# Kernel tuning notes

Hardware: AMD Instinct MI355X
Metric: run time of the kernel (lower is better)

Reference implementation:

```python
import jax, jax.numpy as jnp
import numpy as np

N = 50000      # nodes
E = 800000     # edges (avg degree 16)
IN, H, OUT = 128, 256, 2
BN_EPS = 1e-5


def setup_inputs() -> dict:
    key = jax.random.key(0)
    ks = jax.random.split(key, 24)
    w = lambda k, s: jax.random.normal(k, s, jnp.float32) * 0.05
    inp = {
        "x": jax.random.normal(ks[0], (N, IN), jnp.float32),
        "edge_index": jax.random.randint(ks[1], (2, E), 0, N, jnp.int64),
    }
    # GINConv 1 MLP: Linear(IN,H) -> BN(H) -> ReLU -> Linear(H,H) -> ReLU
    inp.update(c1_W1=w(ks[2], (IN, H)), c1_b1=w(ks[3], (H,)),
               c1_g=jnp.ones((H,), jnp.float32), c1_be=jnp.zeros((H,), jnp.float32),
               c1_W2=w(ks[4], (H, H)), c1_b2=w(ks[5], (H,)))
    # GINConv 2
    inp.update(c2_W1=w(ks[6], (H, H)), c2_b1=w(ks[7], (H,)),
               c2_g=jnp.ones((H,), jnp.float32), c2_be=jnp.zeros((H,), jnp.float32),
               c2_W2=w(ks[8], (H, H)), c2_b2=w(ks[9], (H,)))
    # GINConv 3
    inp.update(c3_W1=w(ks[10], (H, H)), c3_b1=w(ks[11], (H,)),
               c3_g=jnp.ones((H,), jnp.float32), c3_be=jnp.zeros((H,), jnp.float32),
               c3_W2=w(ks[12], (H, H)), c3_b2=w(ks[13], (H,)))
    # readout head
    inp.update(lin1_W=w(ks[14], (3 * H, 3 * H)), lin1_b=w(ks[15], (3 * H,)),
               lin2_W=w(ks[16], (3 * H, OUT)), lin2_b=w(ks[17], (OUT,)))
    return inp


def _gin_conv(x, src, dst, W1, b1, g, be, W2, b2):
    # sum-aggregate neighbor features: agg[i] = sum_{e: dst[e]==i} x[src[e]]
    agg = jax.ops.segment_sum(x[src], dst, num_segments=N)
    h = (x + agg) @ W1 + b1            # (1+eps)*x + agg, eps=0
    mu = h.mean(axis=0)
    var = h.var(axis=0)                # biased var, as torch BN training
    h = jax.nn.relu((h - mu) * jax.lax.rsqrt(var + BN_EPS) * g + be)
    return jax.nn.relu(h @ W2 + b2)


def reference(x, edge_index,
              c1_W1, c1_b1, c1_g, c1_be, c1_W2, c1_b2,
              c2_W1, c2_b1, c2_g, c2_be, c2_W2, c2_b2,
              c3_W1, c3_b1, c3_g, c3_be, c3_W2, c3_b2,
              lin1_W, lin1_b, lin2_W, lin2_b):
    src, dst = edge_index[0], edge_index[1]
    h1 = _gin_conv(x, src, dst, c1_W1, c1_b1, c1_g, c1_be, c1_W2, c1_b2)
    h2 = _gin_conv(h1, src, dst, c2_W1, c2_b1, c2_g, c2_be, c2_W2, c2_b2)
    h3 = _gin_conv(h2, src, dst, c3_W1, c3_b1, c3_g, c3_be, c3_W2, c3_b2)
    h = jnp.concatenate((h1, h2, h3), axis=1)        # [N, 3H]
    h = jax.nn.relu(h @ lin1_W + lin1_b)
    h = h @ lin2_W + lin2_b                          # [N, OUT]
    return h, jax.nn.softmax(h, axis=1)
```

## Files before the change

kernel.cpp:

```cpp
#include <hip/hip_runtime.h>
#include <hip/hip_bf16.h>


#define GIN_N_FEAT_IN 128
#define GIN_H 256
#define M_PAD_ROWS 50176

typedef short short8 __attribute__((ext_vector_type(8)));
typedef float f32x4 __attribute__((ext_vector_type(4)));

#define SCHED_FENCE() __builtin_amdgcn_sched_barrier(0)
#define RAW_BARRIER() __builtin_amdgcn_s_barrier()

__device__ inline ushort f32_to_bf16(float f) {
    union { float f; uint u; } x; x.f = f;
    uint r = x.u + 0x7fff + ((x.u >> 16) & 1);
    return (ushort)(r >> 16);
}
__device__ inline float bf16_to_f32(uint h) {
    union { uint u; float f; } x; x.u = h << 16;
    return x.f;
}
__device__ inline uint pack_bf16(float lo, float hi) {
    return (uint)f32_to_bf16(lo) | ((uint)f32_to_bf16(hi) << 16);
}

__device__ inline void gload_lds16(const ushort* g, ushort* l) {
    __builtin_amdgcn_global_load_lds(
        (const __attribute__((address_space(1))) void*)g,
        (__attribute__((address_space(3))) void*)l, 16, 0, 0);
}


__global__ void cvt_f32_bf16(const float* __restrict__ in, ushort* __restrict__ out, int npairs) {
    for (int i = blockIdx.x * blockDim.x + threadIdx.x; i < npairs; i += gridDim.x * blockDim.x) {
        float2 v = ((const float2*)in)[i];
        ((uint*)out)[i] = pack_bf16(v.x, v.y);
    }
}

struct WPrep {
    const float* src[7];
    ushort* dst[7];
    int R[7];
    int C[7];
};

__global__ void prep_weights(WPrep p) {
    int which = blockIdx.y;
    int R = p.R[which], C = p.C[which];
    int total = R * C;
    const float* src = p.src[which];
    ushort* dst = p.dst[which];
    for (int idx = blockIdx.x * blockDim.x + threadIdx.x; idx < total;
         idx += gridDim.x * blockDim.x) {
        int r = idx / C, c = idx - r * C;
        dst[(size_t)c * R + r] = f32_to_bf16(src[idx]);
    }
}


__global__ void count_kernel(const int* __restrict__ ei, int* __restrict__ deg, int E) {
    for (int e = blockIdx.x * blockDim.x + threadIdx.x; e < E; e += gridDim.x * blockDim.x) {
        atomicAdd(&deg[ei[E + e]], 1);
    }
}

__global__ void scan_chunk(const int* __restrict__ deg, int* __restrict__ row_start,
                           int* __restrict__ chunk_sums, int N) {
    __shared__ int sm[256];
    int tid = threadIdx.x;
    int idx = blockIdx.x * 256 + tid;
    int v = (idx < N) ? deg[idx] : 0;
    sm[tid] = v;
    __syncthreads();
    #pragma unroll
    for (int off = 1; off < 256; off <<= 1) {
        int t = (tid >= off) ? sm[tid - off] : 0;
        __syncthreads();
        sm[tid] += t;
        __syncthreads();
    }
    if (idx < N) row_start[idx] = sm[tid] - v;
    if (tid == 255) chunk_sums[blockIdx.x] = sm[255];
}

__global__ void scan_tops(int* __restrict__ chunk_sums, int* __restrict__ row_start,
                          int nchunks, int N, int E) {
    __shared__ int sm[256];
    int tid = threadIdx.x;
    int v = (tid < nchunks) ? chunk_sums[tid] : 0;
    sm[tid] = v;
    __syncthreads();
    #pragma unroll
    for (int off = 1; off < 256; off <<= 1) {
        int t = (tid >= off) ? sm[tid - off] : 0;
        __syncthreads();
        sm[tid] += t;
        __syncthreads();
    }
    if (tid < nchunks) chunk_sums[tid] = sm[tid] - v;
    if (tid == 0) row_start[N] = E;
}

__global__ void scan_add(int* __restrict__ row_start, int* __restrict__ cursor,
                         const int* __restrict__ chunk_sums, int N) {
    int idx = blockIdx.x * 256 + threadIdx.x;
    if (idx < N) {
        int v = row_start[idx] + chunk_sums[blockIdx.x];
        row_start[idx] = v;
        cursor[idx] = v;
    }
}

__global__ void scatter_kernel(const int* __restrict__ ei, int* __restrict__ cursor,
                               int* __restrict__ perm, int E) {
    for (int e = blockIdx.x * blockDim.x + threadIdx.x; e < E; e += gridDim.x * blockDim.x) {
        int d = ei[E + e];
        int pos = atomicAdd(&cursor[d], 1);
        perm[pos] = ei[e];
    }
}


template <int W>
__global__ void agg2(const ushort* __restrict__ xsrc, int stride,
                     const int* __restrict__ row_start, const int* __restrict__ perm,
                     ushort* __restrict__ out, int N) {
    constexpr int PL = W / 64;
    int node = blockIdx.x * 4 + (threadIdx.x >> 6);
    if (node >= N) return;
    const int lane = threadIdx.x & 63;
    const size_t loff = (size_t)lane * PL;

    float af[PL];
    {
        const ushort* p = xsrc + (size_t)node * stride + loff;
        if constexpr (W == 256) {
            uint2 v = *(const uint2*)p;
            af[0] = bf16_to_f32(v.x & 0xffffu); af[1] = bf16_to_f32(v.x >> 16);
            af[2] = bf16_to_f32(v.y & 0xffffu); af[3] = bf16_to_f32(v.y >> 16);
        } else {
            uint v = *(const uint*)p;
            af[0] = bf16_to_f32(v & 0xffffu); af[1] = bf16_to_f32(v >> 16);
        }
    }
    const int s = row_start[node], e = row_start[node + 1];
    int j = s;
    for (; j + 4 <= e; j += 4) {
        int n0 = perm[j], n1 = perm[j + 1], n2 = perm[j + 2], n3 = perm[j + 3];
        if constexpr (W == 256) {
            uint2 w0 = *(const uint2*)(xsrc + (size_t)n0 * stride + loff);
            uint2 w1 = *(const uint2*)(xsrc + (size_t)n1 * stride + loff);
            uint2 w2 = *(const uint2*)(xsrc + (size_t)n2 * stride + loff);
            uint2 w3 = *(const uint2*)(xsrc + (size_t)n3 * stride + loff);
            af[0] += bf16_to_f32(w0.x & 0xffffu) + bf16_to_f32(w1.x & 0xffffu)
                   + bf16_to_f32(w2.x & 0xffffu) + bf16_to_f32(w3.x & 0xffffu);
            af[1] += bf16_to_f32(w0.x >> 16) + bf16_to_f32(w1.x >> 16)
                   + bf16_to_f32(w2.x >> 16) + bf16_to_f32(w3.x >> 16);
            af[2] += bf16_to_f32(w0.y & 0xffffu) + bf16_to_f32(w1.y & 0xffffu)
                   + bf16_to_f32(w2.y & 0xffffu) + bf16_to_f32(w3.y & 0xffffu);
            af[3] += bf16_to_f32(w0.y >> 16) + bf16_to_f32(w1.y >> 16)
                   + bf16_to_f32(w2.y >> 16) + bf16_to_f32(w3.y >> 16);
        } else {
            uint w0 = *(const uint*)(xsrc + (size_t)n0 * stride + loff);
            uint w1 = *(const uint*)(xsrc + (size_t)n1 * stride + loff);
            uint w2 = *(const uint*)(xsrc + (size_t)n2 * stride + loff);
            uint w3 = *(const uint*)(xsrc + (size_t)n3 * stride + loff);
            af[0] += bf16_to_f32(w0 & 0xffffu) + bf16_to_f32(w1 & 0xffffu)
                   + bf16_to_f32(w2 & 0xffffu) + bf16_to_f32(w3 & 0xffffu);
            af[1] += bf16_to_f32(w0 >> 16) + bf16_to_f32(w1 >> 16)
                   + bf16_to_f32(w2 >> 16) + bf16_to_f32(w3 >> 16);
        }
    }
    for (; j < e; ++j) {
        int sn = perm[j];
        const ushort* p = xsrc + (size_t)sn * stride + loff;
        if constexpr (W == 256) {
            uint2 w = *(const uint2*)p;
            af[0] += bf16_to_f32(w.x & 0xffffu); af[1] += bf16_to_f32(w.x >> 16);
            af[2] += bf16_to_f32(w.y & 0xffffu); af[3] += bf16_to_f32(w.y >> 16);
        } else {
            uint w = *(const uint*)p;
            af[0] += bf16_to_f32(w & 0xffffu); af[1] += bf16_to_f32(w >> 16);
        }
    }
    ushort* po = out + (size_t)node * W + loff;
    if constexpr (W == 256) {
        uint2 o; o.x = pack_bf16(af[0], af[1]); o.y = pack_bf16(af[2], af[3]);
        *(uint2*)po = o;
    } else {
        *(uint*)po = pack_bf16(af[0], af[1]);
    }
}


template <int MODE>
__global__ __launch_bounds__(256) void gemm_mfma(
    const ushort* __restrict__ A, const ushort* __restrict__ Bt,
    const float* __restrict__ bias, void* __restrict__ Cout,
    int ldc, int K, float* __restrict__ extra, int Nvalid) {
    __shared__ ushort As[2][128 * 32];
    __shared__ ushort Bs[2][128 * 32];
    const int tid = threadIdx.x;

    const int gx = gridDim.x;
    const int nwg = gx * gridDim.y;
    const int flat = blockIdx.y * gx + blockIdx.x;
    const int q = nwg >> 3, r = nwg & 7;
    const int xcd = flat & 7, loc = flat >> 3;
    const int wg = (xcd < r ? xcd * (q + 1) : r * (q + 1) + (xcd - r) * q) + loc;
    const int bm = (wg / gx) * 128;
    const int bn = (wg % gx) * 128;

    const int lane = tid & 63;
    const int wid = tid >> 6;
    const int wr = wid >> 1, wc = wid & 1;

    f32x4 acc[4][4] = {};

    const int arow = tid >> 2;
    const int gcol = ((tid & 3) ^ ((tid >> 3) & 3)) * 8;
    const ushort* Ag0 = A + (size_t)(bm + arow) * K + gcol;
    const ushort* Ag1 = A + (size_t)(bm + 64 + arow) * K + gcol;
    const ushort* Bg0 = Bt + (size_t)(bn + arow) * K + gcol;
    const ushort* Bg1 = Bt + (size_t)(bn + 64 + arow) * K + gcol;
    const int wofs = (tid & ~63) * 8;

    const int fr = lane & 15;
    const int rchunk = ((lane >> 4) ^ ((fr >> 1) & 3)) * 8;

    const int NT = K >> 5;

    {
        ushort* a = As[0]; ushort* b = Bs[0];
        gload_lds16(Ag0, a + wofs);
        gload_lds16(Ag1, a + 2048 + wofs);
        gload_lds16(Bg0, b + wofs);
        gload_lds16(Bg1, b + 2048 + wofs);
    }

    for (int it = 0; it < NT; ++it) {
        if (it + 1 < NT) {
            const int k0 = (it + 1) << 5;
            ushort* a = As[(it + 1) & 1]; ushort* b = Bs[(it + 1) & 1];
            gload_lds16(Ag0 + k0, a + wofs);
            gload_lds16(Ag1 + k0, a + 2048 + wofs);
            gload_lds16(Bg0 + k0, b + wofs);
            gload_lds16(Bg1 + k0, b + 2048 + wofs);
            asm volatile("s_waitcnt vmcnt(4)" ::: "memory");
        } else {
            asm volatile("s_waitcnt vmcnt(0)" ::: "memory");
        }
        SCHED_FENCE();
        RAW_BARRIER();

        const ushort* as = As[it & 1];
        const ushort* bs = Bs[it & 1];
        short8 af[4], bf[4];
        #pragma unroll
        for (int m = 0; m < 4; ++m)
            af[m] = *(const short8*)&as[(wr * 64 + m * 16 + fr) * 32 + rchunk];
        #pragma unroll
        for (int n = 0; n < 4; ++n)
            bf[n] = *(const short8*)&bs[(wc * 64 + n * 16 + fr) * 32 + rchunk];
        #pragma unroll
        for (int m = 0; m < 4; ++m)
            #pragma unroll
            for (int n = 0; n < 4; ++n)
                acc[m][n] = __builtin_amdgcn_mfma_f32_16x16x32_bf16(af[m], bf[n], acc[m][n], 0, 0, 0);

        asm volatile("s_waitcnt lgkmcnt(0)" ::: "memory");
        SCHED_FENCE();
        RAW_BARRIER();
    }

    float s1[4], s2[4];
    if constexpr (MODE == 0) {
        #pragma unroll
        for (int n = 0; n < 4; ++n) { s1[n] = 0.f; s2[n] = 0.f; }
    }
    #pragma unroll
    for (int n = 0; n < 4; ++n) {
        const int col = bn + wc * 64 + n * 16 + fr;
        const float bv = bias[col];
        #pragma unroll
        for (int m = 0; m < 4; ++m) {
            const int row0 = bm + wr * 64 + m * 16 + (lane >> 4) * 4;
            #pragma unroll
            for (int rr = 0; rr < 4; ++rr) {
                float v = acc[m][n][rr] + bv;
                if constexpr (MODE == 1) {
                    v = fmaxf(v, 0.f);
                    ((ushort*)Cout)[(size_t)(row0 + rr) * ldc + col] = f32_to_bf16(v);
                } else {
                    ((float*)Cout)[(size_t)(row0 + rr) * ldc + col] = v;
                    if (row0 + rr < Nvalid) { s1[n] += v; s2[n] += v * v; }
                }
            }
        }
    }
    if constexpr (MODE == 0) {
        #pragma unroll
        for (int n = 0; n < 4; ++n) {
            float a = s1[n], b = s2[n];
            a += __shfl_xor(a, 16); b += __shfl_xor(b, 16);
            a += __shfl_xor(a, 32); b += __shfl_xor(b, 32);
            if ((lane >> 4) == 0) {
                int col = bn + wc * 64 + n * 16 + fr;
                atomicAdd(&extra[col], a);
                atomicAdd(&extra[256 + col], b);
            }
        }
    }
}


__global__ __launch_bounds__(512) void gemm_head(
    const ushort* __restrict__ A,
    const ushort* __restrict__ Bt,
    const float* __restrict__ bias,
    const float* __restrict__ w2,
    float* __restrict__ part,
    int K, int MP) {
    __shared__ ushort As[2][256 * 32];
    __shared__ ushort Bs[2][128 * 32];
    __shared__ float sm_part[256][2];
    const int tid = threadIdx.x;

    const int gx = gridDim.x;
    const int nwg = gx * gridDim.y;
    const int flat = blockIdx.y * gx + blockIdx.x;
    const int q = nwg >> 3, r = nwg & 7;
    const int xcd = flat & 7, loc = flat >> 3;
    const int wg = (xcd < r ? xcd * (q + 1) : r * (q + 1) + (xcd - r) * q) + loc;
    const int bm = (wg / gx) * 256;
    const int bn = (wg % gx) * 128;
    const int coltile = wg % gx;

    const int lane = tid & 63;
    const int wid = tid >> 6;
    const int wr = wid >> 1;
    const int wc = wid & 1;

    sm_part[tid >> 1][tid & 1] = 0.f;

    f32x4 acc[4][4] = {};

    const int arow = tid >> 2;
    const int gcol = ((tid & 3) ^ ((tid >> 3) & 3)) * 8;
    const ushort* Ag0 = A + (size_t)(bm + arow) * K + gcol;
    const ushort* Ag1 = A + (size_t)(bm + 128 + arow) * K + gcol;
    const ushort* Bg0 = Bt + (size_t)(bn + arow) * K + gcol;
    const int wofs = (tid & ~63) * 8;

    const int fr = lane & 15;
    const int rchunk = ((lane >> 4) ^ ((fr >> 1) & 3)) * 8;

    const int NT = K >> 5;

    {
        ushort* a = As[0]; ushort* b = Bs[0];
        gload_lds16(Ag0, a + wofs);
        gload_lds16(Ag1, a + 4096 + wofs);
        gload_lds16(Bg0, b + wofs);
    }

    for (int it = 0; it < NT; ++it) {
        if (it + 1 < NT) {
            const int k0 = (it + 1) << 5;
            ushort* a = As[(it + 1) & 1]; ushort* b = Bs[(it + 1) & 1];
            gload_lds16(Ag0 + k0, a + wofs);
            gload_lds16(Ag1 + k0, a + 4096 + wofs);
            gload_lds16(Bg0 + k0, b + wofs);
            asm volatile("s_waitcnt vmcnt(3)" ::: "memory");
        } else {
            asm volatile("s_waitcnt vmcnt(0)" ::: "memory");
        }
        SCHED_FENCE();
        RAW_BARRIER();

        const ushort* as = As[it & 1];
        const ushort* bs = Bs[it & 1];
        short8 af[4], bf[4];
        #pragma unroll
        for (int m = 0; m < 4; ++m)
            af[m] = *(const short8*)&as[(wr * 64 + m * 16 + fr) * 32 + rchunk];
        #pragma unroll
        for (int n = 0; n < 4; ++n)
            bf[n] = *(const short8*)&bs[(wc * 64 + n * 16 + fr) * 32 + rchunk];
        #pragma unroll
        for (int m = 0; m < 4; ++m)
            #pragma unroll
            for (int n = 0; n < 4; ++n)
                acc[m][n] = __builtin_amdgcn_mfma_f32_16x16x32_bf16(af[m], bf[n], acc[m][n], 0, 0, 0);

        asm volatile("s_waitcnt lgkmcnt(0)" ::: "memory");
        SCHED_FENCE();
        RAW_BARRIER();
    }

    #pragma unroll
    for (int m = 0; m < 4; ++m) {
        #pragma unroll
        for (int rr = 0; rr < 4; ++rr) {
            float o0 = 0.f, o1 = 0.f;
            #pragma unroll
            for (int n = 0; n < 4; ++n) {
                int col = bn + wc * 64 + n * 16 + fr;
                float v = fmaxf(acc[m][n][rr] + bias[col], 0.f);
                o0 = fmaf(v, w2[col * 2 + 0], o0);
                o1 = fmaf(v, w2[col * 2 + 1], o1);
            }
            o0 += __shfl_xor(o0, 1); o1 += __shfl_xor(o1, 1);
            o0 += __shfl_xor(o0, 2); o1 += __shfl_xor(o1, 2);
            o0 += __shfl_xor(o0, 4); o1 += __shfl_xor(o1, 4);
            o0 += __shfl_xor(o0, 8); o1 += __shfl_xor(o1, 8);
            if (fr == 0) {
                int lrow = wr * 64 + m * 16 + (lane >> 4) * 4 + rr;
                atomicAdd(&sm_part[lrow][0], o0);
                atomicAdd(&sm_part[lrow][1], o1);
            }
        }
    }
    __syncthreads();
    {
        int lrow = tid >> 1, comp = tid & 1;
        part[((size_t)coltile * MP + bm + lrow) * 2 + comp] = sm_part[lrow][comp];
    }
}


__global__ void bn_apply(const float* __restrict__ h, const float* __restrict__ sums,
                         const float* __restrict__ g, const float* __restrict__ be,
                         ushort* __restrict__ outb, int Nrows) {
    int total = Nrows * 128;
    float inv = 1.0f / (float)Nrows;
    for (int idx = blockIdx.x * blockDim.x + threadIdx.x; idx < total;
         idx += gridDim.x * blockDim.x) {
        int row = idx >> 7;
        int cp = (idx & 127) * 2;
        float2 v = *(const float2*)(h + (size_t)row * 256 + cp);
        float mu0 = sums[cp] * inv,     mu1 = sums[cp + 1] * inv;
        float va0 = sums[256 + cp] * inv - mu0 * mu0;
        float va1 = sums[257 + cp] * inv - mu1 * mu1;
        float o0 = fmaxf((v.x - mu0) * rsqrtf(va0 + 1e-5f) * g[cp]     + be[cp],     0.f);
        float o1 = fmaxf((v.y - mu1) * rsqrtf(va1 + 1e-5f) * g[cp + 1] + be[cp + 1], 0.f);
        *(uint*)(outb + (size_t)row * 256 + cp) = pack_bf16(o0, o1);
    }
}


__global__ void finalize6(const float* __restrict__ part, const float* __restrict__ b2,
                          float* __restrict__ out, int Nrows, int MP) {
    int i = blockIdx.x * blockDim.x + threadIdx.x;
    if (i >= Nrows) return;
    float h0 = b2[0], h1 = b2[1];
    #pragma unroll
    for (int c = 0; c < 6; ++c) {
        h0 += part[((size_t)c * MP + i) * 2 + 0];
        h1 += part[((size_t)c * MP + i) * 2 + 1];
    }
    out[2 * i] = h0;
    out[2 * i + 1] = h1;
    float m = fmaxf(h0, h1);
    float e0 = expf(h0 - m), e1 = expf(h1 - m);
    float s = e0 + e1;
    out[(size_t)2 * Nrows + 2 * i] = e0 / s;
    out[(size_t)2 * Nrows + 2 * i + 1] = e1 / s;
}


extern "C" void kernel_launch(void* const* d_in, const int* in_sizes, int n_in,
                              void* d_out, int out_size, void* d_ws, size_t ws_size,
                              hipStream_t stream) {
    const int N = in_sizes[0] / GIN_N_FEAT_IN;
    const int E = in_sizes[1] / 2;
    const int MP = M_PAD_ROWS;
    const int nchunks = (N + 255) / 256;

    const float* x  = (const float*)d_in[0];
    const int*   ei = (const int*)d_in[1];
    const float* cW1[3] = {(const float*)d_in[2],  (const float*)d_in[8],  (const float*)d_in[14]};
    const float* cb1[3] = {(const float*)d_in[3],  (const float*)d_in[9],  (const float*)d_in[15]};
    const float* cg [3] = {(const float*)d_in[4],  (const float*)d_in[10], (const float*)d_in[16]};
    const float* cbe[3] = {(const float*)d_in[5],  (const float*)d_in[11], (const float*)d_in[17]};
    const float* cW2[3] = {(const float*)d_in[6],  (const float*)d_in[12], (const float*)d_in[18]};
    const float* cb2[3] = {(const float*)d_in[7],  (const float*)d_in[13], (const float*)d_in[19]};
    const float* lin1_W = (const float*)d_in[20];
    const float* lin1_b = (const float*)d_in[21];
    const float* lin2_W = (const float*)d_in[22];
    const float* lin2_b = (const float*)d_in[23];
    float* out = (float*)d_out;

    char* ws = (char*)d_ws;
    size_t off = 0;
    auto carve = [&](size_t bytes) {
        void* p = ws + off;
        off += (bytes + 255) & ~(size_t)255;
        return p;
    };
    ushort* Hcat   = (ushort*)carve((size_t)MP * 768 * 2);
    float*  hlin   = (float*) carve((size_t)MP * 256 * 4);
    ushort* hlin_b = (ushort*)carve((size_t)MP * 256 * 2);
    ushort* hpre   = (ushort*)carve((size_t)MP * 256 * 2);
    ushort* xb     = (ushort*)carve((size_t)MP * 128 * 2);
    ushort* w1t[3] = {(ushort*)carve(256 * 256 * 2), (ushort*)carve(256 * 256 * 2),
                      (ushort*)carve(256 * 256 * 2)};
    ushort* w2t[3] = {(ushort*)carve(256 * 256 * 2), (ushort*)carve(256 * 256 * 2),
                      (ushort*)carve(256 * 256 * 2)};
    ushort* lin1t  = (ushort*)carve((size_t)768 * 768 * 2);
    int*   row_st  = (int*)carve((size_t)(N + 1) * 4);
    int*   cursor  = (int*)carve((size_t)N * 4);
    int*   perm    = (int*)carve((size_t)E * 4);
    int*   csums   = (int*)carve(256 * 4);
    float* bnsums  = (float*)carve(512 * 4);
    float* part    = (float*)carve((size_t)6 * MP * 2 * 4);
    (void)ws_size;

    cvt_f32_bf16<<<1024, 256, 0, stream>>>(x, xb, N * 64);
    WPrep wp;
    wp.src[0] = cW1[0]; wp.dst[0] = w1t[0]; wp.R[0] = 128; wp.C[0] = 256;
    wp.src[1] = cW1[1]; wp.dst[1] = w1t[1]; wp.R[1] = 256; wp.C[1] = 256;
    wp.src[2] = cW1[2]; wp.dst[2] = w1t[2]; wp.R[2] = 256; wp.C[2] = 256;
    wp.src[3] = cW2[0]; wp.dst[3] = w2t[0]; wp.R[3] = 256; wp.C[3] = 256;
    wp.src[4] = cW2[1]; wp.dst[4] = w2t[1]; wp.R[4] = 256; wp.C[4] = 256;
    wp.src[5] = cW2[2]; wp.dst[5] = w2t[2]; wp.R[5] = 256; wp.C[5] = 256;
    wp.src[6] = lin1_W; wp.dst[6] = lin1t;  wp.R[6] = 768; wp.C[6] = 768;
    prep_weights<<<dim3(576, 7), 256, 0, stream>>>(wp);

    hipMemsetAsync(cursor, 0, (size_t)N * 4, stream);
    count_kernel<<<1024, 256, 0, stream>>>(ei, cursor, E);
    scan_chunk<<<nchunks, 256, 0, stream>>>(cursor, row_st, csums, N);
    scan_tops<<<1, 256, 0, stream>>>(csums, row_st, nchunks, N, E);
    scan_add<<<nchunks, 256, 0, stream>>>(row_st, cursor, csums, N);
    scatter_kernel<<<1024, 256, 0, stream>>>(ei, cursor, perm, E);

    const dim3 ggrid(2, MP / 128);
    const int aggblocks = (N + 3) / 4;

    for (int L = 0; L < 3; ++L) {
        if (L == 0)
            agg2<128><<<aggblocks, 256, 0, stream>>>(xb, 128, row_st, perm, hpre, N);
        else
            agg2<256><<<aggblocks, 256, 0, stream>>>(Hcat + (size_t)(L - 1) * 256, 768,
                                                     row_st, perm, hpre, N);

        hipMemsetAsync(bnsums, 0, 512 * 4, stream);
        gemm_mfma<0><<<ggrid, 256, 0, stream>>>(
            hpre, w1t[L], cb1[L], hlin, 256, (L == 0) ? 128 : 256, bnsums, N);

        bn_apply<<<2048, 256, 0, stream>>>(hlin, bnsums, cg[L], cbe[L], hlin_b, N);

        gemm_mfma<1><<<ggrid, 256, 0, stream>>>(
            hlin_b, w2t[L], cb2[L], (void*)(Hcat + (size_t)L * 256), 768, 256,
            nullptr, 0);
    }

    gemm_head<<<dim3(6, MP / 256), 512, 0, stream>>>(
        Hcat, lin1t, lin1_b, lin2_W, part, 768, MP);

    finalize6<<<(N + 255) / 256, 256, 0, stream>>>(part, lin2_b, out, N, MP);
}
```

Before: 673.6 us.

## Triple-buffer LDS tiles in GEMM kernels and raise priority around MFMA

New measurement: 671.5 us. About the same (-0.3%).

```diff
diff --git a/kernel.cpp b/kernel.cpp
--- a/kernel.cpp
+++ b/kernel.cpp
@@ -200,8 +200,8 @@
     const ushort* __restrict__ A, const ushort* __restrict__ Bt,
     const float* __restrict__ bias, void* __restrict__ Cout,
     int ldc, int K, float* __restrict__ extra, int Nvalid) {
-    __shared__ ushort As[2][128 * 32];
-    __shared__ ushort Bs[2][128 * 32];
+    __shared__ ushort As[3][128 * 32];
+    __shared__ ushort Bs[3][128 * 32];
     const int tid = threadIdx.x;
 
     const int gx = gridDim.x;
@@ -232,22 +232,28 @@
 
     const int NT = K >> 5;
 
-    {
-        ushort* a = As[0]; ushort* b = Bs[0];
-        gload_lds16(Ag0, a + wofs);
-        gload_lds16(Ag1, a + 2048 + wofs);
-        gload_lds16(Bg0, b + wofs);
-        gload_lds16(Bg1, b + 2048 + wofs);
-    }
-
+    #pragma unroll
+    for (int t = 0; t < 2; ++t) {
+        const int k0 = t << 5;
+        ushort* a = As[t]; ushort* b = Bs[t];
+        gload_lds16(Ag0 + k0, a + wofs);
+        gload_lds16(Ag1 + k0, a + 2048 + wofs);
+        gload_lds16(Bg0 + k0, b + wofs);
+        gload_lds16(Bg1 + k0, b + 2048 + wofs);
+    }
+
+    int sl = 0;
     for (int it = 0; it < NT; ++it) {
-        if (it + 1 < NT) {
-            const int k0 = (it + 1) << 5;
-            ushort* a = As[(it + 1) & 1]; ushort* b = Bs[(it + 1) & 1];
+        if (it + 2 < NT) {
+            int wsl = sl + 2; if (wsl >= 3) wsl -= 3;
+            const int k0 = (it + 2) << 5;
+            ushort* a = As[wsl]; ushort* b = Bs[wsl];
             gload_lds16(Ag0 + k0, a + wofs);
             gload_lds16(Ag1 + k0, a + 2048 + wofs);
             gload_lds16(Bg0 + k0, b + wofs);
             gload_lds16(Bg1 + k0, b + 2048 + wofs);
+            asm volatile("s_waitcnt vmcnt(8)" ::: "memory");
+        } else if (it + 1 < NT) {
             asm volatile("s_waitcnt vmcnt(4)" ::: "memory");
         } else {
             asm volatile("s_waitcnt vmcnt(0)" ::: "memory");
@@ -255,8 +261,8 @@
         SCHED_FENCE();
         RAW_BARRIER();
 
-        const ushort* as = As[it & 1];
-        const ushort* bs = Bs[it & 1];
+        const ushort* as = As[sl];
+        const ushort* bs = Bs[sl];
         short8 af[4], bf[4];
         #pragma unroll
         for (int m = 0; m < 4; ++m)
@@ -264,15 +270,18 @@
         #pragma unroll
         for (int n = 0; n < 4; ++n)
             bf[n] = *(const short8*)&bs[(wc * 64 + n * 16 + fr) * 32 + rchunk];
+        __builtin_amdgcn_s_setprio(1);
         #pragma unroll
         for (int m = 0; m < 4; ++m)
             #pragma unroll
             for (int n = 0; n < 4; ++n)
                 acc[m][n] = __builtin_amdgcn_mfma_f32_16x16x32_bf16(af[m], bf[n], acc[m][n], 0, 0, 0);
+        __builtin_amdgcn_s_setprio(0);
 
         asm volatile("s_waitcnt lgkmcnt(0)" ::: "memory");
         SCHED_FENCE();
         RAW_BARRIER();
+        sl = sl + 1; if (sl >= 3) sl -= 3;
     }
 
     float s1[4], s2[4];
@@ -323,8 +332,8 @@
     const float* __restrict__ w2,
     float* __restrict__ part,
     int K, int MP) {
-    __shared__ ushort As[2][256 * 32];
-    __shared__ ushort Bs[2][128 * 32];
+    __shared__ ushort As[3][256 * 32];
+    __shared__ ushort Bs[3][128 * 32];
     __shared__ float sm_part[256][2];
     const int tid = threadIdx.x;
 
@@ -359,20 +368,26 @@
 
     const int NT = K >> 5;
 
-    {
-        ushort* a = As[0]; ushort* b = Bs[0];
-        gload_lds16(Ag0, a + wofs);
-        gload_lds16(Ag1, a + 4096 + wofs);
-        gload_lds16(Bg0, b + wofs);
-    }
-
+    #pragma unroll
+    for (int t = 0; t < 2; ++t) {
+        const int k0 = t << 5;
+        ushort* a = As[t]; ushort* b = Bs[t];
+        gload_lds16(Ag0 + k0, a + wofs);
+        gload_lds16(Ag1 + k0, a + 4096 + wofs);
+        gload_lds16(Bg0 + k0, b + wofs);
+    }
+
+    int sl = 0;
     for (int it = 0; it < NT; ++it) {
-        if (it + 1 < NT) {
-            const int k0 = (it + 1) << 5;
-            ushort* a = As[(it + 1) & 1]; ushort* b = Bs[(it + 1) & 1];
+        if (it + 2 < NT) {
+            int wsl = sl + 2; if (wsl >= 3) wsl -= 3;
+            const int k0 = (it + 2) << 5;
+            ushort* a = As[wsl]; ushort* b = Bs[wsl];
             gload_lds16(Ag0 + k0, a + wofs);
             gload_lds16(Ag1 + k0, a + 4096 + wofs);
             gload_lds16(Bg0 + k0, b + wofs);
+            asm volatile("s_waitcnt vmcnt(6)" ::: "memory");
+        } else if (it + 1 < NT) {
             asm volatile("s_waitcnt vmcnt(3)" ::: "memory");
         } else {
             asm volatile("s_waitcnt vmcnt(0)" ::: "memory");
@@ -380,8 +395,8 @@
         SCHED_FENCE();
         RAW_BARRIER();
 
-        const ushort* as = As[it & 1];
-        const ushort* bs = Bs[it & 1];
+        const ushort* as = As[sl];
+        const ushort* bs = Bs[sl];
         short8 af[4], bf[4];
         #pragma unroll
         for (int m = 0; m < 4; ++m)
@@ -389,15 +404,18 @@
         #pragma unroll
         for (int n = 0; n < 4; ++n)
             bf[n] = *(const short8*)&bs[(wc * 64 + n * 16 + fr) * 32 + rchunk];
+        __builtin_amdgcn_s_setprio(1);
         #pragma unroll
         for (int m = 0; m < 4; ++m)
             #pragma unroll
             for (int n = 0; n < 4; ++n)
                 acc[m][n] = __builtin_amdgcn_mfma_f32_16x16x32_bf16(af[m], bf[n], acc[m][n], 0, 0, 0);
+        __builtin_amdgcn_s_setprio(0);
 
         asm volatile("s_waitcnt lgkmcnt(0)" ::: "memory");
         SCHED_FENCE();
         RAW_BARRIER();
+        sl = sl + 1; if (sl >= 3) sl -= 3;
     }
 
     #pragma unroll
```
